# Performance work log

Hardware: AMD Instinct MI355X
Metric: run time of the kernel (lower is better)

The kernel has to match this reference:

```python
import jax, jax.numpy as jnp
import numpy as np

SCALE_MIN, SCALE_MAX = 0.01, 10.0
LN_EPS = 1e-5

B, KIN, H, C = 32, 6144, 512, 5


def _kaiming_uniform(k, shape):
    # torch kaiming_uniform_(a=sqrt(5)) on (out,in): bound = 1/sqrt(fan_in)
    bound = 1.0 / np.sqrt(shape[1])
    return jax.random.uniform(k, shape, minval=-bound, maxval=bound, dtype=jnp.float32)


def setup_inputs() -> dict:
    key = jax.random.key(0)
    ks = jax.random.split(key, 16)
    inp = {"x": jax.random.normal(ks[0], (B, KIN), dtype=jnp.float32)}
    dims = [(H, KIN), (H, H), (H, H)]
    for i, (o, n) in enumerate(dims):
        inp[f"w{i}"] = _kaiming_uniform(ks[1 + 3 * i], (o, n))
        inp[f"t{i}"] = jax.random.uniform(ks[2 + 3 * i], (o, n), minval=-1.0, maxval=1.0, dtype=jnp.float32)
        inp[f"s{i}"] = jax.random.uniform(ks[3 + 3 * i], (o, n), minval=-2.0, maxval=0.0, dtype=jnp.float32)
        inp[f"g{i}"] = jnp.ones((o,), jnp.float32)
        inp[f"b{i}"] = jnp.zeros((o,), jnp.float32)
    inp["cw"] = _kaiming_uniform(ks[10], (C, H))
    cbound = 1.0 / np.sqrt(H)
    inp["cb"] = jax.random.uniform(ks[11], (C,), minval=-cbound, maxval=cbound, dtype=jnp.float32)
    return inp


def _wavelet_linear(h, w, t, sr):
    # h: (B, in), params: (out, in)
    scale = SCALE_MIN + (SCALE_MAX - SCALE_MIN) * jax.nn.sigmoid(sr)
    s = (h[:, None, :] - t[None]) / (scale[None] + 1e-8)  # (B, out, in)
    psi = (1.0 - s * s) * jnp.exp(-0.5 * s * s)  # mexican hat
    return jnp.einsum('boi,oi->bo', psi, w)


def _layer_norm(h, g, b):
    m = jnp.mean(h, axis=-1, keepdims=True)
    v = jnp.mean(jnp.square(h - m), axis=-1, keepdims=True)
    return (h - m) * jax.lax.rsqrt(v + LN_EPS) * g + b


def reference(x, w0, t0, s0, g0, b0, w1, t1, s1, g1, b1, w2, t2, s2, g2, b2, cw, cb):
    h = x
    for (w, t, sr, g, b) in [(w0, t0, s0, g0, b0), (w1, t1, s1, g1, b1), (w2, t2, s2, g2, b2)]:
        h = _layer_norm(jax.nn.silu(_wavelet_linear(h, w, t, sr)), g, b)
    return h @ cw.T + cb
```

## Files before the change

### kernel.cpp

```cpp
#include <hip/hip_runtime.h>

#define LN_EPS 1e-5f
#define LOG2E 1.44269504f
#define NHALF_LOG2E (-0.72134752f)

#if __has_builtin(__builtin_amdgcn_exp2f)
#define EXP2F(x) __builtin_amdgcn_exp2f(x)
#else
#define EXP2F(x) __expf((x) * 0.69314718f)
#endif

typedef float v2f __attribute__((ext_vector_type(2)));

template<int KIN>
__global__ __launch_bounds__(256)
void transpose_x(const float* __restrict__ x, float* __restrict__ xT)
{
    int idx = blockIdx.x * 256 + threadIdx.x;
    int i = idx >> 5, b = idx & 31;
    xT[idx] = x[b * KIN + i];
}

template<int KIN, int S, int NO>
__global__ __launch_bounds__(128, 4)
void wav_layer(const float* __restrict__ xT, const float* __restrict__ w,
               const float* __restrict__ t, const float* __restrict__ s,
               float* __restrict__ part)
{
    constexpr int RANGE = KIN / S;
    constexpr int STEPS = RANGE / 4;
    __shared__ float2 prepA[2][NO][RANGE];
    __shared__ float  prepW[2][NO][RANGE];

    const int wave  = threadIdx.x >> 6;
    const int lane  = threadIdx.x & 63;
    const int obase = ((blockIdx.x << 1) + wave) * NO;
    const int si    = blockIdx.y;
    const int ibase = si * RANGE;

#pragma unroll
    for (int e = lane; e < NO * RANGE; e += 64) {
        int ol = e / RANGE, il = e - ol * RANGE;
        size_t gi = (size_t)(obase + ol) * KIN + ibase + il;
        float wv = w[gi], tv = t[gi], sv = s[gi];
        float sig = __builtin_amdgcn_rcpf(1.f + EXP2F(-sv * LOG2E));
        float inv = __builtin_amdgcn_rcpf(fmaf(9.99f, sig, 0.01000001f));
        prepA[wave][ol][il] = make_float2(inv, -tv * inv);
        prepW[wave][ol][il] = wv;
    }
    __syncthreads();

    const int p = lane & 15, g = lane >> 4;
    const v2f* __restrict__ xp = (const v2f*)xT + (size_t)(ibase + g) * 16 + p;

    v2f xr[STEPS];
#pragma unroll
    for (int st = 0; st < STEPS; ++st) xr[st] = xp[(size_t)st * 64];

#pragma unroll
    for (int ol = 0; ol < NO; ++ol) {
        v2f acc = {0.f, 0.f};
#pragma unroll
        for (int st = 0; st < STEPS; ++st) {
            float2 pr = prepA[wave][ol][st * 4 + g];
            float  wj = prepW[wave][ol][st * 4 + g];
            v2f u  = __builtin_elementwise_fma(xr[st], (v2f){pr.x, pr.x},
                                               (v2f){pr.y, pr.y});
            v2f q  = u * u;
            v2f ev = {EXP2F(q.x * NHALF_LOG2E), EXP2F(q.y * NHALF_LOG2E)};
            v2f pw = __builtin_elementwise_fma((v2f){-wj, -wj}, q,
                                               (v2f){wj, wj});
            acc = __builtin_elementwise_fma(pw, ev, acc);
        }
        float a0 = acc.x, a1 = acc.y;
        a0 += __shfl_down(a0, 32); a0 += __shfl_down(a0, 16);
        a1 += __shfl_down(a1, 32); a1 += __shfl_down(a1, 16);
        if (lane < 16) {
            float2* pp = (float2*)(part + (size_t)si * 16384 + (obase + ol) * 32) + p;
            *pp = make_float2(a0, a1);
        }
    }
}

template<int S>
__global__ __launch_bounds__(512)
void silu_ln(const float* __restrict__ part, const float* __restrict__ g,
             const float* __restrict__ bias, float* __restrict__ hT)
{
    const int b = blockIdx.x, tid = threadIdx.x;
    float v = 0.f;
#pragma unroll
    for (int si = 0; si < S; ++si) v += part[(size_t)si * 16384 + tid * 32 + b];
    float a = v * __builtin_amdgcn_rcpf(1.f + EXP2F(-v * LOG2E));

    float s1 = a, s2 = a * a;
#pragma unroll
    for (int off = 32; off; off >>= 1) {
        s1 += __shfl_down(s1, off);
        s2 += __shfl_down(s2, off);
    }
    __shared__ float r1[8], r2[8];
    const int lane = tid & 63, wid = tid >> 6;
    if (lane == 0) { r1[wid] = s1; r2[wid] = s2; }
    __syncthreads();
    float t1 = 0.f, t2 = 0.f;
#pragma unroll
    for (int k = 0; k < 8; ++k) { t1 += r1[k]; t2 += r2[k]; }
    float m   = t1 * (1.f / 512.f);
    float var = t2 * (1.f / 512.f) - m * m;
    float r   = __builtin_amdgcn_rsqf(var + LN_EPS);
    hT[tid * 32 + b] = (a - m) * r * g[tid] + bias[tid];
}

template<int S>
__global__ __launch_bounds__(512)
void silu_ln_cls(const float* __restrict__ part, const float* __restrict__ g,
                 const float* __restrict__ bias, const float* __restrict__ cw,
                 const float* __restrict__ cb, float* __restrict__ out)
{
    const int b = blockIdx.x, tid = threadIdx.x;
    float v = 0.f;
#pragma unroll
    for (int si = 0; si < S; ++si) v += part[(size_t)si * 16384 + tid * 32 + b];
    float a = v * __builtin_amdgcn_rcpf(1.f + EXP2F(-v * LOG2E));

    float s1 = a, s2 = a * a;
#pragma unroll
    for (int off = 32; off; off >>= 1) {
        s1 += __shfl_down(s1, off);
        s2 += __shfl_down(s2, off);
    }
    __shared__ float r1[8], r2[8];
    const int lane = tid & 63, wid = tid >> 6;
    if (lane == 0) { r1[wid] = s1; r2[wid] = s2; }
    __syncthreads();
    float t1 = 0.f, t2 = 0.f;
#pragma unroll
    for (int k = 0; k < 8; ++k) { t1 += r1[k]; t2 += r2[k]; }
    float m   = t1 * (1.f / 512.f);
    float var = t2 * (1.f / 512.f) - m * m;
    float r   = __builtin_amdgcn_rsqf(var + LN_EPS);
    float hl  = (a - m) * r * g[tid] + bias[tid];

    __shared__ float cr[5][8];
#pragma unroll
    for (int c = 0; c < 5; ++c) {
        float pv = hl * cw[c * 512 + tid];
#pragma unroll
        for (int off = 32; off; off >>= 1) pv += __shfl_down(pv, off);
        if (lane == 0) cr[c][wid] = pv;
    }
    __syncthreads();
    if (tid < 5) {
        float sum = 0.f;
#pragma unroll
        for (int k = 0; k < 8; ++k) sum += cr[tid][k];
        out[b * 5 + tid] = sum + cb[tid];
    }
}

extern "C" void kernel_launch(void* const* d_in, const int* in_sizes, int n_in,
                              void* d_out, int out_size, void* d_ws, size_t ws_size,
                              hipStream_t stream)
{
    const float* x  = (const float*)d_in[0];
    const float* w0 = (const float*)d_in[1];
    const float* t0 = (const float*)d_in[2];
    const float* s0 = (const float*)d_in[3];
    const float* g0 = (const float*)d_in[4];
    const float* b0 = (const float*)d_in[5];
    const float* w1 = (const float*)d_in[6];
    const float* t1 = (const float*)d_in[7];
    const float* s1 = (const float*)d_in[8];
    const float* g1 = (const float*)d_in[9];
    const float* b1 = (const float*)d_in[10];
    const float* w2 = (const float*)d_in[11];
    const float* t2 = (const float*)d_in[12];
    const float* s2 = (const float*)d_in[13];
    const float* g2 = (const float*)d_in[14];
    const float* b2 = (const float*)d_in[15];
    const float* cw = (const float*)d_in[16];
    const float* cb = (const float*)d_in[17];
    float* out = (float*)d_out;

    float* xT   = (float*)d_ws;
    float* part = xT + 196608;
    float* hT   = part + 64 * 16384;

    transpose_x<6144><<<768, 256, 0, stream>>>(x, xT);
    wav_layer<6144, 64, 8><<<dim3(32, 64), 128, 0, stream>>>(xT, w0, t0, s0, part);
    silu_ln<64><<<32, 512, 0, stream>>>(part, g0, b0, hT);
    wav_layer<512, 16, 4><<<dim3(64, 16), 128, 0, stream>>>(hT, w1, t1, s1, part);
    silu_ln<16><<<32, 512, 0, stream>>>(part, g1, b1, hT);
    wav_layer<512, 16, 4><<<dim3(64, 16), 128, 0, stream>>>(hT, w2, t2, s2, part);
    silu_ln_cls<16><<<32, 512, 0, stream>>>(part, g2, b2, cw, cb, out);
}
```

Baseline: 196.9 us.

## Fuse all layers into one persistent kernel with software grid barriers

Replaces the seven-kernel chain with a single persistent launch of 1024 blocks that runs the transpose, three wavelet stages, and the LayerNorm and classifier stages, separated by atomic-counter grid barriers. The goal is to remove per-launch overhead and tail gaps between small kernels. Layer 0 now uses 16 outputs per wave with 1024 blocks instead of 2048, and the partial-sum layout is changed to batch-major so LN can use float4 loads. It relies on all 1024 blocks being co-resident, with a spin guard that could let a barrier fall through. Most blocks also sit idle during the LN stages.

```diff
diff --git a/kernel.cpp b/kernel.cpp
--- a/kernel.cpp
+++ b/kernel.cpp
@@ -3,6 +3,8 @@
 #define LN_EPS 1e-5f
 #define LOG2E 1.44269504f
 #define NHALF_LOG2E (-0.72134752f)
+#define NBLK 1024
+#define SPIN_GUARD (1 << 20)
 
 #if __has_builtin(__builtin_amdgcn_exp2f)
 #define EXP2F(x) __builtin_amdgcn_exp2f(x)
@@ -12,31 +14,68 @@
 
 typedef float v2f __attribute__((ext_vector_type(2)));
 
-template<int KIN>
-__global__ __launch_bounds__(256)
-void transpose_x(const float* __restrict__ x, float* __restrict__ xT)
-{
-    int idx = blockIdx.x * 256 + threadIdx.x;
-    int i = idx >> 5, b = idx & 31;
-    xT[idx] = x[b * KIN + i];
-}
+__device__ __forceinline__ float silu_f(float v) {
+    return v * __builtin_amdgcn_rcpf(1.f + EXP2F(-v * LOG2E));
+}
+
+__global__ __launch_bounds__(576)
+void init_ctr(int* __restrict__ ctr)
+{
+    ctr[blockIdx.x * 576 + threadIdx.x] = 0;
+}
+
+__device__ __forceinline__ void grid_barrier(int* base, int bx, int tid)
+{
+    __threadfence();
+    __syncthreads();
+    if (tid == 0) {
+        atomicAdd(&base[(bx & 31) << 4], 1);
+        if (bx == 0) {
+            int guard = 0;
+            for (;;) {
+                int tot = 0;
+#pragma unroll
+                for (int j = 0; j < 32; ++j)
+                    tot += __hip_atomic_load(&base[j << 4], __ATOMIC_RELAXED,
+                                             __HIP_MEMORY_SCOPE_AGENT);
+                if (tot >= NBLK || ++guard > SPIN_GUARD) break;
+            }
+            __threadfence();
+            __hip_atomic_store(&base[512], 1, __ATOMIC_RELEASE,
+                               __HIP_MEMORY_SCOPE_AGENT);
+        } else {
+            int guard = 0;
+            while (__hip_atomic_load(&base[512], __ATOMIC_ACQUIRE,
+                                     __HIP_MEMORY_SCOPE_AGENT) == 0) {
+                if (++guard > SPIN_GUARD) break;
+                __builtin_amdgcn_s_sleep(2);
+            }
+        }
+    }
+    __syncthreads();
+}
+
+union SharedU {
+    struct { float2 A[2][16][96]; float W[2][16][96]; } p0;
+    struct { float2 A[2][4][32];  float W[2][4][32];  } p1;
+    struct { float r1[2], r2[2], cr[5][2]; } red;
+};
 
 template<int KIN, int S, int NO>
-__global__ __launch_bounds__(128, 4)
-void wav_layer(const float* __restrict__ xT, const float* __restrict__ w,
-               const float* __restrict__ t, const float* __restrict__ s,
-               float* __restrict__ part)
+__device__ __forceinline__ void wav_stage(int bx, int wave, int lane,
+    const float* __restrict__ xT, const float* __restrict__ w,
+    const float* __restrict__ t, const float* __restrict__ s,
+    float* __restrict__ part, float2* prepA, float* prepW)
 {
     constexpr int RANGE = KIN / S;
     constexpr int STEPS = RANGE / 4;
-    __shared__ float2 prepA[2][NO][RANGE];
-    __shared__ float  prepW[2][NO][RANGE];
-
-    const int wave  = threadIdx.x >> 6;
-    const int lane  = threadIdx.x & 63;
-    const int obase = ((blockIdx.x << 1) + wave) * NO;
-    const int si    = blockIdx.y;
+    constexpr int OGRP = 512 / (2 * NO);
+    const int og = bx % OGRP;
+    const int si = bx / OGRP;
+    const int obase = (og * 2 + wave) * NO;
     const int ibase = si * RANGE;
+    float2* pA = prepA + wave * (NO * RANGE);
+    float*  pW = prepW + wave * (NO * RANGE);
 
 #pragma unroll
     for (int e = lane; e < NO * RANGE; e += 64) {
@@ -45,25 +84,23 @@
         float wv = w[gi], tv = t[gi], sv = s[gi];
         float sig = __builtin_amdgcn_rcpf(1.f + EXP2F(-sv * LOG2E));
         float inv = __builtin_amdgcn_rcpf(fmaf(9.99f, sig, 0.01000001f));
-        prepA[wave][ol][il] = make_float2(inv, -tv * inv);
-        prepW[wave][ol][il] = wv;
+        pA[ol * RANGE + il] = make_float2(inv, -tv * inv);
+        pW[ol * RANGE + il] = wv;
     }
     __syncthreads();
 
     const int p = lane & 15, g = lane >> 4;
     const v2f* __restrict__ xp = (const v2f*)xT + (size_t)(ibase + g) * 16 + p;
-
     v2f xr[STEPS];
 #pragma unroll
     for (int st = 0; st < STEPS; ++st) xr[st] = xp[(size_t)st * 64];
 
-#pragma unroll
     for (int ol = 0; ol < NO; ++ol) {
         v2f acc = {0.f, 0.f};
 #pragma unroll
         for (int st = 0; st < STEPS; ++st) {
-            float2 pr = prepA[wave][ol][st * 4 + g];
-            float  wj = prepW[wave][ol][st * 4 + g];
+            float2 pr = pA[ol * RANGE + st * 4 + g];
+            float  wj = pW[ol * RANGE + st * 4 + g];
             v2f u  = __builtin_elementwise_fma(xr[st], (v2f){pr.x, pr.x},
                                                (v2f){pr.y, pr.y});
             v2f q  = u * u;
@@ -76,87 +113,143 @@
         a0 += __shfl_down(a0, 32); a0 += __shfl_down(a0, 16);
         a1 += __shfl_down(a1, 32); a1 += __shfl_down(a1, 16);
         if (lane < 16) {
-            float2* pp = (float2*)(part + (size_t)si * 16384 + (obase + ol) * 32) + p;
-            *pp = make_float2(a0, a1);
+            float* bp = part + (size_t)si * 16384 + obase + ol;
+            bp[(2 * p) * 512]     = a0;
+            bp[(2 * p + 1) * 512] = a1;
         }
     }
 }
 
 template<int S>
-__global__ __launch_bounds__(512)
-void silu_ln(const float* __restrict__ part, const float* __restrict__ g,
-             const float* __restrict__ bias, float* __restrict__ hT)
-{
-    const int b = blockIdx.x, tid = threadIdx.x;
-    float v = 0.f;
-#pragma unroll
-    for (int si = 0; si < S; ++si) v += part[(size_t)si * 16384 + tid * 32 + b];
-    float a = v * __builtin_amdgcn_rcpf(1.f + EXP2F(-v * LOG2E));
-
-    float s1 = a, s2 = a * a;
+__device__ __forceinline__ void ln_stage(int b, int tid,
+    const float* __restrict__ part, const float* __restrict__ g,
+    const float* __restrict__ bias, float* __restrict__ hT,
+    float* r1, float* r2)
+{
+    const int o0 = tid * 4;
+    float v0 = 0.f, v1 = 0.f, v2 = 0.f, v3 = 0.f;
+#pragma unroll
+    for (int si = 0; si < S; ++si) {
+        float4 pv = *(const float4*)(part + (size_t)si * 16384 + b * 512 + o0);
+        v0 += pv.x; v1 += pv.y; v2 += pv.z; v3 += pv.w;
+    }
+    float a0 = silu_f(v0), a1 = silu_f(v1), a2 = silu_f(v2), a3 = silu_f(v3);
+    float s1 = a0 + a1 + a2 + a3;
+    float s2 = a0*a0 + a1*a1 + a2*a2 + a3*a3;
 #pragma unroll
     for (int off = 32; off; off >>= 1) {
         s1 += __shfl_down(s1, off);
         s2 += __shfl_down(s2, off);
     }
-    __shared__ float r1[8], r2[8];
     const int lane = tid & 63, wid = tid >> 6;
     if (lane == 0) { r1[wid] = s1; r2[wid] = s2; }
     __syncthreads();
-    float t1 = 0.f, t2 = 0.f;
-#pragma unroll
-    for (int k = 0; k < 8; ++k) { t1 += r1[k]; t2 += r2[k]; }
+    float t1 = r1[0] + r1[1], t2 = r2[0] + r2[1];
     float m   = t1 * (1.f / 512.f);
     float var = t2 * (1.f / 512.f) - m * m;
     float r   = __builtin_amdgcn_rsqf(var + LN_EPS);
-    hT[tid * 32 + b] = (a - m) * r * g[tid] + bias[tid];
+    hT[(o0 + 0) * 32 + b] = (a0 - m) * r * g[o0 + 0] + bias[o0 + 0];
+    hT[(o0 + 1) * 32 + b] = (a1 - m) * r * g[o0 + 1] + bias[o0 + 1];
+    hT[(o0 + 2) * 32 + b] = (a2 - m) * r * g[o0 + 2] + bias[o0 + 2];
+    hT[(o0 + 3) * 32 + b] = (a3 - m) * r * g[o0 + 3] + bias[o0 + 3];
 }
 
 template<int S>
-__global__ __launch_bounds__(512)
-void silu_ln_cls(const float* __restrict__ part, const float* __restrict__ g,
-                 const float* __restrict__ bias, const float* __restrict__ cw,
-                 const float* __restrict__ cb, float* __restrict__ out)
-{
-    const int b = blockIdx.x, tid = threadIdx.x;
-    float v = 0.f;
-#pragma unroll
-    for (int si = 0; si < S; ++si) v += part[(size_t)si * 16384 + tid * 32 + b];
-    float a = v * __builtin_amdgcn_rcpf(1.f + EXP2F(-v * LOG2E));
-
-    float s1 = a, s2 = a * a;
+__device__ __forceinline__ void cls_stage(int b, int tid,
+    const float* __restrict__ part, const float* __restrict__ g,
+    const float* __restrict__ bias, const float* __restrict__ cw,
+    const float* __restrict__ cb, float* __restrict__ out,
+    float* r1, float* r2, float* cr)
+{
+    const int o0 = tid * 4;
+    float v0 = 0.f, v1 = 0.f, v2 = 0.f, v3 = 0.f;
+#pragma unroll
+    for (int si = 0; si < S; ++si) {
+        float4 pv = *(const float4*)(part + (size_t)si * 16384 + b * 512 + o0);
+        v0 += pv.x; v1 += pv.y; v2 += pv.z; v3 += pv.w;
+    }
+    float a0 = silu_f(v0), a1 = silu_f(v1), a2 = silu_f(v2), a3 = silu_f(v3);
+    float s1 = a0 + a1 + a2 + a3;
+    float s2 = a0*a0 + a1*a1 + a2*a2 + a3*a3;
 #pragma unroll
     for (int off = 32; off; off >>= 1) {
         s1 += __shfl_down(s1, off);
         s2 += __shfl_down(s2, off);
     }
-    __shared__ float r1[8], r2[8];
     const int lane = tid & 63, wid = tid >> 6;
     if (lane == 0) { r1[wid] = s1; r2[wid] = s2; }
     __syncthreads();
-    float t1 = 0.f, t2 = 0.f;
-#pragma unroll
-    for (int k = 0; k < 8; ++k) { t1 += r1[k]; t2 += r2[k]; }
+    float t1 = r1[0] + r1[1], t2 = r2[0] + r2[1];
     float m   = t1 * (1.f / 512.f);
     float var = t2 * (1.f / 512.f) - m * m;
     float r   = __builtin_amdgcn_rsqf(var + LN_EPS);
-    float hl  = (a - m) * r * g[tid] + bias[tid];
-
-    __shared__ float cr[5][8];
+    float h0 = (a0 - m) * r * g[o0 + 0] + bias[o0 + 0];
+    float h1 = (a1 - m) * r * g[o0 + 1] + bias[o0 + 1];
+    float h2 = (a2 - m) * r * g[o0 + 2] + bias[o0 + 2];
+    float h3 = (a3 - m) * r * g[o0 + 3] + bias[o0 + 3];
 #pragma unroll
     for (int c = 0; c < 5; ++c) {
-        float pv = hl * cw[c * 512 + tid];
+        const float* cwr = cw + c * 512 + o0;
+        float pv = h0 * cwr[0] + h1 * cwr[1] + h2 * cwr[2] + h3 * cwr[3];
 #pragma unroll
         for (int off = 32; off; off >>= 1) pv += __shfl_down(pv, off);
-        if (lane == 0) cr[c][wid] = pv;
-    }
-    __syncthreads();
-    if (tid < 5) {
-        float sum = 0.f;
-#pragma unroll
-        for (int k = 0; k < 8; ++k) sum += cr[tid][k];
-        out[b * 5 + tid] = sum + cb[tid];
-    }
+        if (lane == 0) cr[c * 2 + wid] = pv;
+    }
+    __syncthreads();
+    if (tid < 5) out[b * 5 + tid] = cr[tid * 2] + cr[tid * 2 + 1] + cb[tid];
+}
+
+__global__ __launch_bounds__(128, 4)
+void fused(const float* __restrict__ x,
+           const float* __restrict__ w0, const float* __restrict__ t0,
+           const float* __restrict__ s0, const float* __restrict__ g0,
+           const float* __restrict__ b0,
+           const float* __restrict__ w1, const float* __restrict__ t1,
+           const float* __restrict__ s1, const float* __restrict__ g1,
+           const float* __restrict__ b1,
+           const float* __restrict__ w2, const float* __restrict__ t2,
+           const float* __restrict__ s2, const float* __restrict__ g2,
+           const float* __restrict__ b2,
+           const float* __restrict__ cw, const float* __restrict__ cb,
+           float* __restrict__ out,
+           float* __restrict__ xT, float* __restrict__ pA,
+           float* __restrict__ pB, float* __restrict__ pC,
+           float* __restrict__ hT, float* __restrict__ h2T,
+           int* __restrict__ ctr)
+{
+    __shared__ SharedU sh;
+    const int bx   = blockIdx.x;
+    const int tid  = threadIdx.x;
+    const int wave = tid >> 6, lane = tid & 63;
+
+    {
+        int idx = bx * 128 + tid;
+        xT[idx] = x[(idx & 31) * 6144 + (idx >> 5)];
+        int idx2 = idx + 131072;
+        if (idx2 < 196608) xT[idx2] = x[(idx2 & 31) * 6144 + (idx2 >> 5)];
+    }
+    grid_barrier(ctr + 0 * 576, bx, tid);
+
+    wav_stage<6144, 64, 16>(bx, wave, lane, xT, w0, t0, s0, pA,
+                            &sh.p0.A[0][0][0], &sh.p0.W[0][0][0]);
+    grid_barrier(ctr + 1 * 576, bx, tid);
+
+    if (bx < 32) ln_stage<64>(bx, tid, pA, g0, b0, hT, sh.red.r1, sh.red.r2);
+    grid_barrier(ctr + 2 * 576, bx, tid);
+
+    wav_stage<512, 16, 4>(bx, wave, lane, hT, w1, t1, s1, pB,
+                          &sh.p1.A[0][0][0], &sh.p1.W[0][0][0]);
+    grid_barrier(ctr + 3 * 576, bx, tid);
+
+    if (bx < 32) ln_stage<16>(bx, tid, pB, g1, b1, h2T, sh.red.r1, sh.red.r2);
+    grid_barrier(ctr + 4 * 576, bx, tid);
+
+    wav_stage<512, 16, 4>(bx, wave, lane, h2T, w2, t2, s2, pC,
+                          &sh.p1.A[0][0][0], &sh.p1.W[0][0][0]);
+    grid_barrier(ctr + 5 * 576, bx, tid);
+
+    if (bx < 32) cls_stage<16>(bx, tid, pC, g2, b2, cw, cb, out,
+                               sh.red.r1, sh.red.r2, &sh.red.cr[0][0]);
 }
 
 extern "C" void kernel_launch(void* const* d_in, const int* in_sizes, int n_in,
@@ -183,15 +276,18 @@
     const float* cb = (const float*)d_in[17];
     float* out = (float*)d_out;
 
-    float* xT   = (float*)d_ws;
-    float* part = xT + 196608;
-    float* hT   = part + 64 * 16384;
-
-    transpose_x<6144><<<768, 256, 0, stream>>>(x, xT);
-    wav_layer<6144, 64, 8><<<dim3(32, 64), 128, 0, stream>>>(xT, w0, t0, s0, part);
-    silu_ln<64><<<32, 512, 0, stream>>>(part, g0, b0, hT);
-    wav_layer<512, 16, 4><<<dim3(64, 16), 128, 0, stream>>>(hT, w1, t1, s1, part);
-    silu_ln<16><<<32, 512, 0, stream>>>(part, g1, b1, hT);
-    wav_layer<512, 16, 4><<<dim3(64, 16), 128, 0, stream>>>(hT, w2, t2, s2, part);
-    silu_ln_cls<16><<<32, 512, 0, stream>>>(part, g2, b2, cw, cb, out);
-}
+    int*   ctr = (int*)d_ws;
+    float* xT  = (float*)d_ws + 4096;
+    float* pA  = xT + 196608;
+    float* pB  = pA + 64 * 16384;
+    float* pC  = pB + 16 * 16384;
+    float* hT  = pC + 16 * 16384;
+    float* h2T = hT + 16384;
+
+    init_ctr<<<6, 576, 0, stream>>>(ctr);
+    fused<<<NBLK, 128, 0, stream>>>(x, w0, t0, s0, g0, b0,
+                                    w1, t1, s1, g1, b1,
+                                    w2, t2, s2, g2, b2,
+                                    cw, cb, out,
+                                    xT, pA, pB, pC, hT, h2T, ctr);
+}
```

Measured after the change: 689.1 us. +250.0%, slower.
